# Kernel tuning notes

Measured on AMD Instinct MI355X. Metric: run time of the kernel, lower is better.

The kernel has to match this reference:

```python
import jax, jax.numpy as jnp
import numpy as np

N_NODES = 100000
N_EDGES = 1600000
NODE_NF = 11   # num_node_fs
EDGE_NF = 4    # edges_nf
H_NF = 128     # h_nf
EMB_NF = 4     # emb_nf


def _linear_params(k, fan_in, fan_out):
    # torch nn.Linear default init: U(-1/sqrt(fan_in), 1/sqrt(fan_in))
    lim = 1.0 / np.sqrt(fan_in)
    kw, kb = jax.random.split(k)
    W = jax.random.uniform(kw, (fan_in, fan_out), minval=-lim, maxval=lim, dtype=jnp.float32)
    b = jax.random.uniform(kb, (fan_out,), minval=-lim, maxval=lim, dtype=jnp.float32)
    return W, b


def setup_inputs() -> dict:
    key = jax.random.key(0)
    ks = jax.random.split(key, 8)
    node_feats = jax.random.normal(ks[0], (N_NODES, NODE_NF), dtype=jnp.float32)
    edge_index = jax.random.randint(ks[1], (2, N_EDGES), 0, N_NODES, dtype=jnp.int32)
    edge_attr = jax.random.normal(ks[2], (N_EDGES, EDGE_NF), dtype=jnp.float32)
    # NELayer edge MLP: Linear(2*in_nf+edges_nf, h_nf) -> ReLU -> Linear(h_nf, h_nf) -> ReLU
    eW1, eb1 = _linear_params(ks[3], 2 * NODE_NF + EDGE_NF, H_NF)
    eW2, eb2 = _linear_params(ks[4], H_NF, H_NF)
    # NELayer node MLP: Linear(in_nf+h_nf, h_nf) -> ReLU -> Linear(h_nf, out_nf=h_nf)
    nW1, nb1 = _linear_params(ks[5], NODE_NF + H_NF, H_NF)
    nW2, nb2 = _linear_params(ks[6], H_NF, H_NF)
    # fc_emb: Linear(h_nf, emb_nf)
    fW, fb = _linear_params(ks[7], H_NF, EMB_NF)
    return dict(node_feats=node_feats, edge_index=edge_index, edge_attr=edge_attr,
                eW1=eW1, eb1=eb1, eW2=eW2, eb2=eb2,
                nW1=nW1, nb1=nb1, nW2=nW2, nb2=nb2, fW=fW, fb=fb)


def reference(node_feats, edge_index, edge_attr,
              eW1, eb1, eW2, eb2, nW1, nb1, nW2, nb2, fW, fb):
    row, col = edge_index[0], edge_index[1]          # [E], [E]
    src = node_feats[row]                            # [E, NODE_NF] gather
    dst = node_feats[col]                            # [E, NODE_NF] gather
    # edge model
    e_in = jnp.concatenate([src, dst, edge_attr], axis=1)   # [E, 2*NODE_NF+EDGE_NF]
    e_h = jax.nn.relu(e_in @ eW1 + eb1)
    edge_feats = jax.nn.relu(e_h @ eW2 + eb2)                # [E, H_NF]
    # node model: scatter-sum edge feats to source nodes
    agg = jax.ops.segment_sum(edge_feats, row, num_segments=node_feats.shape[0])  # [N, H_NF]
    n_in = jnp.concatenate([node_feats, agg], axis=1)        # [N, NODE_NF+H_NF]
    n_h = jax.nn.relu(n_in @ nW1 + nb1)
    h = n_h @ nW2 + nb2                                      # [N, H_NF]
    # embedding head
    return h @ fW + fb                                       # [N, EMB_NF]
```

## Files before the change

kernel.cpp:

```cpp
#include <hip/hip_runtime.h>

#define N_NODES 100000
#define N_EDGES 1600000
#define NODE_NF 11
#define EDGE_NF 4
#define H_NF 128
#define SCAN_B 1024
#define NBLK ((N_NODES + SCAN_B - 1) / SCAN_B)

#define ASP 32
#define K1P 40
#define K2P 136
#define EFP 131
#define K1N 160

typedef _Float16 half8 __attribute__((ext_vector_type(8)));
typedef float floatx4 __attribute__((ext_vector_type(4)));

__device__ inline half8 load8f(const float* p) {
    float4 x0 = *(const float4*)(p);
    float4 x1 = *(const float4*)(p + 4);
    half8 r;
    r[0]=(_Float16)x0.x; r[1]=(_Float16)x0.y; r[2]=(_Float16)x0.z; r[3]=(_Float16)x0.w;
    r[4]=(_Float16)x1.x; r[5]=(_Float16)x1.y; r[6]=(_Float16)x1.z; r[7]=(_Float16)x1.w;
    return r;
}
__device__ inline half8 zero8() {
    half8 z;
    #pragma unroll
    for (int j = 0; j < 8; ++j) z[j] = (_Float16)0.f;
    return z;
}

#define SEG0 (N_NODES * 12)
#define SEG1 (SEG0 + H_NF * K1P)
#define SEG2 (SEG1 + H_NF * K2P)
#define SEG3 (SEG2 + H_NF * K1N)
#define SEG4 (SEG3 + 16 * K2P + 4)
#define SEG5 (SEG4 + N_EDGES)

__global__ __launch_bounds__(256)
void prep_hist_kernel(const float* __restrict__ nf,
                      const float* __restrict__ eW1,
                      const float* __restrict__ eW2,
                      const float* __restrict__ nW1,
                      const float* __restrict__ nW2,
                      const float* __restrict__ fW,
                      const float* __restrict__ nb2,
                      const float* __restrict__ fb,
                      const int*   __restrict__ edge_index,
                      _Float16* __restrict__ nfh,
                      _Float16* __restrict__ w1h,
                      _Float16* __restrict__ w2h,
                      _Float16* __restrict__ w1nh,
                      _Float16* __restrict__ w23h,
                      float* __restrict__ b23,
                      int* hist)
{
    int i = blockIdx.x * 256 + threadIdx.x;
    if (i < SEG0) {
        int n = i / 12, k = i - n * 12;
        nfh[i] = (k < NODE_NF) ? (_Float16)nf[(size_t)n * NODE_NF + k] : (_Float16)0.f;
    } else if (i < SEG1) {
        int j = i - SEG0;
        int n = j / K1P, k = j - n * K1P;
        float v = 0.f;
        if (k < 11)                 v = eW1[k * H_NF + n];
        else if (k >= 12 && k < 23) v = eW1[(k - 1) * H_NF + n];
        else if (k >= 24 && k < 28) v = eW1[(k - 2) * H_NF + n];
        w1h[j] = (_Float16)v;
    } else if (i < SEG2) {
        int j = i - SEG1;
        int n = j / K2P, k = j - n * K2P;
        w2h[j] = (k < H_NF) ? (_Float16)eW2[k * H_NF + n] : (_Float16)0.f;
    } else if (i < SEG3) {
        int j = i - SEG2;
        int n = j / K1N, k = j - n * K1N;
        float v = 0.f;
        if (k < 11)                  v = nW1[k * H_NF + n];
        else if (k >= 12 && k < 140) v = nW1[(k - 1) * H_NF + n];
        w1nh[j] = (_Float16)v;
    } else if (i < SEG4) {
        int j = i - SEG3;
        if (j < 16 * K2P) {
            int n = j / K2P, k = j - n * K2P;
            float v = 0.f;
            if (n < 4 && k < H_NF) {
                for (int q = 0; q < H_NF; ++q) v += nW2[k * H_NF + q] * fW[q * 4 + n];
            }
            w23h[j] = (_Float16)v;
        } else {
            int o = j - 16 * K2P;
            float v = fb[o];
            for (int q = 0; q < H_NF; ++q) v += nb2[q] * fW[q * 4 + o];
            b23[o] = v;
        }
    } else if (i < SEG5) {
        int e = i - SEG4;
        atomicAdd(&hist[edge_index[e]], 1);
    }
}

__global__ __launch_bounds__(256)
void transpose_w2(const float* __restrict__ W, float* __restrict__ WT) {
    int i = blockIdx.x * 256 + threadIdx.x;
    if (i < H_NF * H_NF) {
        int k = i >> 7, j = i & (H_NF - 1);
        WT[j * H_NF + k] = W[i];
    }
}

__global__ __launch_bounds__(SCAN_B)
void scan1_kernel(const int* __restrict__ hist, int* starts, int* bsum) {
    __shared__ int buf[SCAN_B];
    int i = blockIdx.x * SCAN_B + threadIdx.x;
    int v = (i < N_NODES) ? hist[i] : 0;
    buf[threadIdx.x] = v;
    __syncthreads();
    for (int off = 1; off < SCAN_B; off <<= 1) {
        int t = (threadIdx.x >= off) ? buf[threadIdx.x - off] : 0;
        __syncthreads();
        buf[threadIdx.x] += t;
        __syncthreads();
    }
    if (i < N_NODES) starts[i] = buf[threadIdx.x] - v;
    if (threadIdx.x == SCAN_B - 1) bsum[blockIdx.x] = buf[SCAN_B - 1];
}

__global__ void scan2_kernel(int* bsum) {
    if (threadIdx.x == 0 && blockIdx.x == 0) {
        int run = 0;
        for (int b = 0; b < NBLK; ++b) { int t = bsum[b]; bsum[b] = run; run += t; }
        bsum[NBLK] = run;
    }
}

__global__ __launch_bounds__(256)
void scan3_kernel(int* starts, int* cursor, const int* __restrict__ bsum) {
    int i = blockIdx.x * 256 + threadIdx.x;
    if (i < N_NODES) {
        int s = starts[i] + bsum[i / SCAN_B];
        starts[i] = s;
        cursor[i] = s;
    }
    if (i == 0) starts[N_NODES] = bsum[NBLK];
}

__global__ __launch_bounds__(256)
void permgather_kernel(const int* __restrict__ edge_index,
                       const _Float16* __restrict__ nfh,
                       const float* __restrict__ edge_attr,
                       int* cursor,
                       _Float16* __restrict__ Asort,
                       int* __restrict__ rows_sorted)
{
    int e = blockIdx.x * 256 + threadIdx.x;
    if (e >= N_EDGES) return;
    int row = edge_index[e];
    int col = edge_index[N_EDGES + e];
    int pos = atomicAdd(&cursor[row], 1);
    rows_sorted[pos] = row;
    const int2* ps = (const int2*)(nfh + (size_t)row * 12);
    const int2* pd = (const int2*)(nfh + (size_t)col * 12);
    int2 s0 = ps[0], s1 = ps[1], s2 = ps[2];
    int2 d0 = pd[0], d1 = pd[1], d2 = pd[2];
    float4 a4 = ((const float4*)edge_attr)[e];
    union { _Float16 h[4]; int2 v; } u;
    u.h[0] = (_Float16)a4.x; u.h[1] = (_Float16)a4.y;
    u.h[2] = (_Float16)a4.z; u.h[3] = (_Float16)a4.w;
    int2* op = (int2*)(Asort + (size_t)pos * ASP);
    op[0] = s0; op[1] = s1; op[2] = s2;
    op[3] = d0; op[4] = d1; op[5] = d2;
    op[6] = u.v; op[7] = make_int2(0, 0);
}

__global__ __launch_bounds__(256)
void permute_kernel(const int* __restrict__ edge_index, int* cursor, int* perm) {
    int e = blockIdx.x * 256 + threadIdx.x;
    if (e < N_EDGES) {
        int pos = atomicAdd(&cursor[edge_index[e]], 1);
        perm[pos] = e;
    }
}

#define E_ARENA_SZ 4480

__global__ __launch_bounds__(256, 2)
void edge_mfma_kernel(const _Float16* __restrict__ Asort,
                      const int*   __restrict__ rows_sorted,
                      const _Float16* __restrict__ w1h,
                      const float* __restrict__ eb1,
                      const _Float16* __restrict__ w2h,
                      const float* __restrict__ eb2,
                      float* agg)
{
    __shared__ __align__(16) char smem[4 * E_ARENA_SZ];
    int t = threadIdx.x;
    int wv = t >> 6, lane = t & 63;
    char* arena = smem + wv * E_ARENA_SZ;
    _Float16* Hs = (_Float16*)arena;
    int* rowsS = (int*)(arena + 4352);
    int m = lane & 15, quad = lane >> 4;

    half8 w1f[8], w2f[8][4];
    #pragma unroll
    for (int tile = 0; tile < 8; ++tile)
        w1f[tile] = *(const half8*)(w1h + (tile * 16 + m) * K1P + quad * 8);
    #pragma unroll
    for (int tile = 0; tile < 8; ++tile)
        #pragma unroll
        for (int ks = 0; ks < 4; ++ks)
            w2f[tile][ks] = *(const half8*)(w2h + (tile * 16 + m) * K2P + ks * 32 + quad * 8);
    float b1v[8], b2v[8];
    #pragma unroll
    for (int tile = 0; tile < 8; ++tile) {
        b1v[tile] = eb1[tile * 16 + m];
        b2v[tile] = eb2[tile * 16 + m];
    }

    const int nwin = N_EDGES / 16;
    const int STRIDE = gridDim.x * 4;
    int win = blockIdx.x * 4 + wv;
    if (win >= nwin) return;

    half8 a1 = *(const half8*)(Asort + (size_t)win * (16 * ASP) + m * ASP + quad * 8);
    int rs = (quad == 3) ? rows_sorted[win * 16 + m] : 0;

    while (true) {
        int next = win + STRIDE;
        bool hn = next < nwin;
        if (quad == 3) rowsS[m] = rs;
        half8 a1n = {};
        int rsn = 0;
        if (hn) {
            a1n = *(const half8*)(Asort + (size_t)next * (16 * ASP) + m * ASP + quad * 8);
            if (quad == 3) rsn = rows_sorted[next * 16 + m];
        }

        #pragma unroll
        for (int tile = 0; tile < 8; ++tile) {
            floatx4 c = {0.f, 0.f, 0.f, 0.f};
            c = __builtin_amdgcn_mfma_f32_16x16x32_f16(a1, w1f[tile], c, 0, 0, 0);
            int n = tile * 16 + m;
            #pragma unroll
            for (int r = 0; r < 4; ++r)
                Hs[(quad * 4 + r) * K2P + n] = (_Float16)fmaxf(c[r] + b1v[tile], 0.f);
        }

        half8 a2[4];
        #pragma unroll
        for (int ks = 0; ks < 4; ++ks)
            a2[ks] = *(const half8*)(Hs + m * K2P + ks * 32 + quad * 8);

        float vals[32];
        #pragma unroll
        for (int tile = 0; tile < 8; ++tile) {
            floatx4 c = {0.f, 0.f, 0.f, 0.f};
            #pragma unroll
            for (int ks = 0; ks < 4; ++ks)
                c = __builtin_amdgcn_mfma_f32_16x16x32_f16(a2[ks], w2f[tile][ks], c, 0, 0, 0);
            #pragma unroll
            for (int r = 0; r < 4; ++r)
                vals[tile * 4 + r] = fmaxf(c[r] + b2v[tile], 0.f);
        }

        int er0 = rowsS[quad * 4 + 0], er1 = rowsS[quad * 4 + 1];
        int er2 = rowsS[quad * 4 + 2], er3 = rowsS[quad * 4 + 3];
        int li = lane & 15;
        bool bi = (lane < 16) && ((li == 0) || (rowsS[li] != rowsS[li - 1]));
        unsigned long long bm = __ballot(bi);
        unsigned mk = (unsigned)(bm & 0xFFFFull);
        while (mk) {
            int start = __builtin_ctz(mk);
            mk &= mk - 1;
            int srow = rowsS[start];
            float s[8];
            #pragma unroll
            for (int tile = 0; tile < 8; ++tile) {
                float v = 0.f;
                if (er0 == srow) v += vals[tile * 4 + 0];
                if (er1 == srow) v += vals[tile * 4 + 1];
                if (er2 == srow) v += vals[tile * 4 + 2];
                if (er3 == srow) v += vals[tile * 4 + 3];
                s[tile] = v;
            }
            #pragma unroll
            for (int tile = 0; tile < 8; ++tile) {
                s[tile] += __shfl_xor(s[tile], 16);
                s[tile] += __shfl_xor(s[tile], 32);
            }
            if (quad == 0) {
                #pragma unroll
                for (int tile = 0; tile < 8; ++tile)
                    unsafeAtomicAdd(&agg[(size_t)srow * H_NF + tile * 16 + m], s[tile]);
            }
        }

        if (!hn) break;
        win = next; a1 = a1n; rs = rsn;
    }
}

#define G_W1      0
#define G_W2      10240
#define G_ARENA   45056
#define G_ARENA_SZ 8448
#define G_TOTAL   (G_ARENA + 4 * G_ARENA_SZ)

__global__ __launch_bounds__(256, 2)
void edge_mfma_gather_kernel(const _Float16* __restrict__ nfh,
                             const int*   __restrict__ edge_index,
                             const float* __restrict__ edge_attr,
                             const _Float16* __restrict__ w1h,
                             const float* __restrict__ eb1,
                             const _Float16* __restrict__ w2h,
                             const float* __restrict__ eb2,
                             const int*   __restrict__ perm,
                             float* agg)
{
    __shared__ __align__(16) char smem[G_TOTAL];
    _Float16* W1s = (_Float16*)(smem + G_W1);
    _Float16* W2s = (_Float16*)(smem + G_W2);
    int t = threadIdx.x;
    {
        const float4* g1 = (const float4*)w1h;
        float4* s1 = (float4*)W1s;
        for (int i = t; i < 640; i += 256) s1[i] = g1[i];
        const float4* g2 = (const float4*)w2h;
        float4* s2 = (float4*)W2s;
        for (int i = t; i < 2176; i += 256) s2[i] = g2[i];
    }
    __syncthreads();

    int wv = t >> 6, lane = t & 63;
    char* arena = smem + G_ARENA + wv * G_ARENA_SZ;
    _Float16* Ain  = (_Float16*)arena;
    _Float16* Hs   = (_Float16*)(arena + 1280);
    float*    efS  = (float*)arena;
    int*      rowsS = (int*)(arena + 8384);

    int m = lane & 15, quad = lane >> 4;
    int el = lane & 15, grp = lane >> 4;
    _Float16* arow = Ain + el * K1P;

    float b1v[8], b2v[8];
    #pragma unroll
    for (int tile = 0; tile < 8; ++tile) {
        b1v[tile] = eb1[tile * 16 + m];
        b2v[tile] = eb2[tile * 16 + m];
    }

    const int nwin = N_EDGES / 16;
    for (int win = blockIdx.x * 4 + wv; win < nwin; win += gridDim.x * 4) {
        int e = perm[win * 16 + el];
        if (grp < 2) {
            int node = edge_index[grp * N_EDGES + e];
            const int2* p = (const int2*)(nfh + (size_t)node * 12);
            int2 x0 = p[0], x1 = p[1], x2 = p[2];
            char* dst = (char*)(arow + grp * 12);
            *(int2*)(dst) = x0; *(int2*)(dst + 8) = x1; *(int2*)(dst + 16) = x2;
        } else if (grp == 2) {
            float4 a4 = ((const float4*)edge_attr)[e];
            arow[24] = (_Float16)a4.x; arow[25] = (_Float16)a4.y;
            arow[26] = (_Float16)a4.z; arow[27] = (_Float16)a4.w;
        } else {
            rowsS[el] = edge_index[e];
            *(int2*)((char*)arow + 56) = make_int2(0, 0);
        }

        half8 a1 = *(const half8*)(Ain + m * K1P + quad * 8);
        #pragma unroll
        for (int tile = 0; tile < 8; ++tile) {
            half8 b = *(const half8*)(W1s + (tile * 16 + m) * K1P + quad * 8);
            floatx4 c = {0.f, 0.f, 0.f, 0.f};
            c = __builtin_amdgcn_mfma_f32_16x16x32_f16(a1, b, c, 0, 0, 0);
            int n = tile * 16 + m;
            #pragma unroll
            for (int r = 0; r < 4; ++r)
                Hs[(quad * 4 + r) * K2P + n] = (_Float16)fmaxf(c[r] + b1v[tile], 0.f);
        }
        half8 a2[4];
        #pragma unroll
        for (int ks = 0; ks < 4; ++ks)
            a2[ks] = *(const half8*)(Hs + m * K2P + ks * 32 + quad * 8);
        #pragma unroll
        for (int tile = 0; tile < 8; ++tile) {
            floatx4 c = {0.f, 0.f, 0.f, 0.f};
            #pragma unroll
            for (int ks = 0; ks < 4; ++ks) {
                half8 b = *(const half8*)(W2s + (tile * 16 + m) * K2P + ks * 32 + quad * 8);
                c = __builtin_amdgcn_mfma_f32_16x16x32_f16(a2[ks], b, c, 0, 0, 0);
            }
            #pragma unroll
            for (int r = 0; r < 4; ++r)
                efS[(quad * 4 + r) * EFP + tile * 16 + m] = fmaxf(c[r] + b2v[tile], 0.f);
        }

        int f = lane;
        int cur = rowsS[0];
        float acc0 = efS[f], acc1 = efS[64 + f];
        #pragma unroll 1
        for (int i = 1; i < 16; ++i) {
            int r = rowsS[i];
            float v0 = efS[i * EFP + f];
            float v1 = efS[i * EFP + 64 + f];
            if (r != cur) {
                unsafeAtomicAdd(&agg[(size_t)cur * H_NF + f], acc0);
                unsafeAtomicAdd(&agg[(size_t)cur * H_NF + 64 + f], acc1);
                acc0 = v0; acc1 = v1; cur = r;
            } else { acc0 += v0; acc1 += v1; }
        }
        unsafeAtomicAdd(&agg[(size_t)cur * H_NF + f], acc0);
        unsafeAtomicAdd(&agg[(size_t)cur * H_NF + 64 + f], acc1);
    }
}

#define N_W1    0
#define N_W23   40960
#define N_HS    45312

__global__ __launch_bounds__(256, 2)
void node_mfma_kernel(const float* __restrict__ node_feats,
                      const float* __restrict__ agg,
                      const _Float16* __restrict__ w1nh,
                      const float* __restrict__ nb1,
                      const _Float16* __restrict__ w23h,
                      const float* __restrict__ b23,
                      float* __restrict__ out)
{
    __shared__ __align__(16) char smem[N_HS + 4 * 4352];
    _Float16* W1N  = (_Float16*)(smem + N_W1);
    _Float16* W23s = (_Float16*)(smem + N_W23);
    int t = threadIdx.x;
    {
        const float4* g1 = (const float4*)w1nh;
        float4* s1 = (float4*)W1N;
        for (int i = t; i < 2560; i += 256) s1[i] = g1[i];
        const float4* g2 = (const float4*)w23h;
        float4* s2 = (float4*)W23s;
        for (int i = t; i < 272; i += 256) s2[i] = g2[i];
    }
    __syncthreads();

    int wv = t >> 6, lane = t & 63;
    int m = lane & 15, quad = lane >> 4;
    _Float16* HsW = (_Float16*)(smem + N_HS + wv * 4352);
    const int ntile = (N_NODES + 63) / 64;

    float nb1v[8];
    #pragma unroll
    for (int tile = 0; tile < 8; ++tile) nb1v[tile] = nb1[tile * 16 + m];
    float b23v = (m < 4) ? b23[m] : 0.f;

    for (int ti = blockIdx.x; ti < ntile; ti += gridDim.x) {
        int nb = (ti * 4 + wv) * 16;
        if (nb >= N_NODES) continue;
        int nodeA = nb + m;
        if (nodeA >= N_NODES) nodeA = N_NODES - 1;
        const float* ag  = agg + (size_t)nodeA * H_NF;
        const float* nfp = node_feats + (size_t)nodeA * NODE_NF;

        half8 afr[5];
        if (quad == 0) {
            half8 r;
            #pragma unroll
            for (int j = 0; j < 8; ++j) r[j] = (_Float16)nfp[j];
            afr[0] = r;
            afr[4] = load8f(ag + 116);
        } else if (quad == 1) {
            half8 r;
            r[0] = (_Float16)nfp[8]; r[1] = (_Float16)nfp[9];
            r[2] = (_Float16)nfp[10]; r[3] = (_Float16)0.f;
            float4 x = *(const float4*)(ag);
            r[4] = (_Float16)x.x; r[5] = (_Float16)x.y;
            r[6] = (_Float16)x.z; r[7] = (_Float16)x.w;
            afr[0] = r;
            float4 y = *(const float4*)(ag + 124);
            half8 s = zero8();
            s[0] = (_Float16)y.x; s[1] = (_Float16)y.y;
            s[2] = (_Float16)y.z; s[3] = (_Float16)y.w;
            afr[4] = s;
        } else if (quad == 2) {
            afr[0] = load8f(ag + 4);
            afr[4] = zero8();
        } else {
            afr[0] = load8f(ag + 12);
            afr[4] = zero8();
        }
        afr[1] = load8f(ag + 20 + 8 * quad);
        afr[2] = load8f(ag + 52 + 8 * quad);
        afr[3] = load8f(ag + 84 + 8 * quad);

        #pragma unroll
        for (int tile = 0; tile < 8; ++tile) {
            floatx4 c = {0.f, 0.f, 0.f, 0.f};
            #pragma unroll
            for (int ks = 0; ks < 5; ++ks) {
                half8 b = *(const half8*)(W1N + (tile * 16 + m) * K1N + ks * 32 + quad * 8);
                c = __builtin_amdgcn_mfma_f32_16x16x32_f16(afr[ks], b, c, 0, 0, 0);
            }
            #pragma unroll
            for (int r = 0; r < 4; ++r)
                HsW[(quad * 4 + r) * K2P + tile * 16 + m] = (_Float16)fmaxf(c[r] + nb1v[tile], 0.f);
        }

        half8 a2[4];
        #pragma unroll
        for (int ks = 0; ks < 4; ++ks)
            a2[ks] = *(const half8*)(HsW + m * K2P + ks * 32 + quad * 8);
        floatx4 c23 = {0.f, 0.f, 0.f, 0.f};
        #pragma unroll
        for (int ks = 0; ks < 4; ++ks) {
            half8 b = *(const half8*)(W23s + m * K2P + ks * 32 + quad * 8);
            c23 = __builtin_amdgcn_mfma_f32_16x16x32_f16(a2[ks], b, c23, 0, 0, 0);
        }
        if (m < 4) {
            #pragma unroll
            for (int r = 0; r < 4; ++r) {
                int node = nb + quad * 4 + r;
                if (node < N_NODES) out[node * 4 + m] = c23[r] + b23v;
            }
        }
    }
}

__global__ __launch_bounds__(256)
void edge_kernel_atomic(const float* __restrict__ node_feats,
                        const int*   __restrict__ edge_index,
                        const float* __restrict__ edge_attr,
                        const float* __restrict__ eW1,
                        const float* __restrict__ eb1,
                        const float* __restrict__ W2T,
                        const float* __restrict__ eb2,
                        float* agg)
{
    int e = blockIdx.x * 256 + threadIdx.x;
    if (e >= N_EDGES) return;
    int row = edge_index[e];
    int col = edge_index[N_EDGES + e];
    float h[H_NF];
    #pragma unroll
    for (int j = 0; j < H_NF; ++j) h[j] = eb1[j];
    const float* srcp = node_feats + (size_t)row * NODE_NF;
    #pragma unroll 1
    for (int k = 0; k < NODE_NF; ++k) {
        float x = srcp[k];
        const float* w = eW1 + k * H_NF;
        #pragma unroll
        for (int j = 0; j < H_NF; ++j) h[j] = fmaf(x, w[j], h[j]);
    }
    const float* dstp = node_feats + (size_t)col * NODE_NF;
    #pragma unroll 1
    for (int k = 0; k < NODE_NF; ++k) {
        float x = dstp[k];
        const float* w = eW1 + (NODE_NF + k) * H_NF;
        #pragma unroll
        for (int j = 0; j < H_NF; ++j) h[j] = fmaf(x, w[j], h[j]);
    }
    float4 at = ((const float4*)edge_attr)[e];
    float av[EDGE_NF] = {at.x, at.y, at.z, at.w};
    #pragma unroll
    for (int k = 0; k < EDGE_NF; ++k) {
        float x = av[k];
        const float* w = eW1 + (2 * NODE_NF + k) * H_NF;
        #pragma unroll
        for (int j = 0; j < H_NF; ++j) h[j] = fmaf(x, w[j], h[j]);
    }
    #pragma unroll
    for (int j = 0; j < H_NF; ++j) h[j] = fmaxf(h[j], 0.f);
    #pragma unroll 1
    for (int j0 = 0; j0 < H_NF; j0 += 8) {
        float acc[8];
        #pragma unroll
        for (int jj = 0; jj < 8; ++jj) acc[jj] = eb2[j0 + jj];
        #pragma unroll
        for (int k = 0; k < H_NF; ++k) {
            float x = h[k];
            #pragma unroll
            for (int jj = 0; jj < 8; ++jj)
                acc[jj] = fmaf(x, W2T[(j0 + jj) * H_NF + k], acc[jj]);
        }
        #pragma unroll
        for (int jj = 0; jj < 8; ++jj)
            unsafeAtomicAdd(&agg[(size_t)row * H_NF + j0 + jj], fmaxf(acc[jj], 0.f));
    }
}

__global__ __launch_bounds__(256)
void node_kernel1(const float* __restrict__ node_feats, float* agg_nh,
                  const float* __restrict__ nW1, const float* __restrict__ nb1)
{
    int n = blockIdx.x * 256 + threadIdx.x;
    if (n >= N_NODES) return;
    float acc[H_NF];
    #pragma unroll
    for (int j = 0; j < H_NF; ++j) acc[j] = nb1[j];
    const float* nfp = node_feats + (size_t)n * NODE_NF;
    #pragma unroll 1
    for (int k = 0; k < NODE_NF; ++k) {
        float x = nfp[k];
        const float* w = nW1 + k * H_NF;
        #pragma unroll
        for (int j = 0; j < H_NF; ++j) acc[j] = fmaf(x, w[j], acc[j]);
    }
    const float4* ap = (const float4*)(agg_nh + (size_t)n * H_NF);
    #pragma unroll 1
    for (int k4 = 0; k4 < H_NF / 4; ++k4) {
        float4 x = ap[k4];
        const float* w0 = nW1 + (NODE_NF + k4 * 4 + 0) * H_NF;
        const float* w1 = nW1 + (NODE_NF + k4 * 4 + 1) * H_NF;
        const float* w2 = nW1 + (NODE_NF + k4 * 4 + 2) * H_NF;
        const float* w3 = nW1 + (NODE_NF + k4 * 4 + 3) * H_NF;
        #pragma unroll
        for (int j = 0; j < H_NF; ++j) {
            acc[j] = fmaf(x.x, w0[j], acc[j]);
            acc[j] = fmaf(x.y, w1[j], acc[j]);
            acc[j] = fmaf(x.z, w2[j], acc[j]);
            acc[j] = fmaf(x.w, w3[j], acc[j]);
        }
    }
    float* op = agg_nh + (size_t)n * H_NF;
    #pragma unroll
    for (int j4 = 0; j4 < H_NF / 4; ++j4) {
        float4 o = make_float4(fmaxf(acc[j4*4+0], 0.f), fmaxf(acc[j4*4+1], 0.f),
                               fmaxf(acc[j4*4+2], 0.f), fmaxf(acc[j4*4+3], 0.f));
        ((float4*)op)[j4] = o;
    }
}

__global__ __launch_bounds__(256)
void node_kernel2(const float* __restrict__ nh, const float* __restrict__ nW2,
                  const float* __restrict__ nb2, const float* __restrict__ fW,
                  const float* __restrict__ fb, float* __restrict__ out)
{
    int n = blockIdx.x * 256 + threadIdx.x;
    if (n >= N_NODES) return;
    float acc[H_NF];
    #pragma unroll
    for (int j = 0; j < H_NF; ++j) acc[j] = nb2[j];
    const float4* hp = (const float4*)(nh + (size_t)n * H_NF);
    #pragma unroll 1
    for (int k4 = 0; k4 < H_NF / 4; ++k4) {
        float4 x = hp[k4];
        const float* w0 = nW2 + (k4 * 4 + 0) * H_NF;
        const float* w1 = nW2 + (k4 * 4 + 1) * H_NF;
        const float* w2 = nW2 + (k4 * 4 + 2) * H_NF;
        const float* w3 = nW2 + (k4 * 4 + 3) * H_NF;
        #pragma unroll
        for (int j = 0; j < H_NF; ++j) {
            acc[j] = fmaf(x.x, w0[j], acc[j]);
            acc[j] = fmaf(x.y, w1[j], acc[j]);
            acc[j] = fmaf(x.z, w2[j], acc[j]);
            acc[j] = fmaf(x.w, w3[j], acc[j]);
        }
    }
    float o0 = fb[0], o1 = fb[1], o2 = fb[2], o3 = fb[3];
    #pragma unroll
    for (int j = 0; j < H_NF; ++j) {
        o0 = fmaf(acc[j], fW[j * 4 + 0], o0);
        o1 = fmaf(acc[j], fW[j * 4 + 1], o1);
        o2 = fmaf(acc[j], fW[j * 4 + 2], o2);
        o3 = fmaf(acc[j], fW[j * 4 + 3], o3);
    }
    ((float4*)out)[n] = make_float4(o0, o1, o2, o3);
}

extern "C" void kernel_launch(void* const* d_in, const int* in_sizes, int n_in,
                              void* d_out, int out_size, void* d_ws, size_t ws_size,
                              hipStream_t stream)
{
    const float* node_feats = (const float*)d_in[0];
    const int*   edge_index = (const int*)d_in[1];
    const float* edge_attr  = (const float*)d_in[2];
    const float* eW1 = (const float*)d_in[3];
    const float* eb1 = (const float*)d_in[4];
    const float* eW2 = (const float*)d_in[5];
    const float* eb2 = (const float*)d_in[6];
    const float* nW1 = (const float*)d_in[7];
    const float* nb1 = (const float*)d_in[8];
    const float* nW2 = (const float*)d_in[9];
    const float* nb2 = (const float*)d_in[10];
    const float* fW  = (const float*)d_in[11];
    const float* fb  = (const float*)d_in[12];
    float* out = (float*)d_out;

    size_t off = 0;
    auto carve = [&](size_t bytes) {
        void* p = (char*)d_ws + off;
        off = (off + bytes + 255) & ~(size_t)255;
        return p;
    };
    float*     agg    = (float*)carve((size_t)N_NODES * H_NF * sizeof(float));
    int*       hist   = (int*)  carve((size_t)N_NODES * sizeof(int));
    size_t zero_bytes = off;
    int*       starts = (int*)  carve((size_t)(N_NODES + 1) * sizeof(int));
    int*       cursor = (int*)  carve((size_t)N_NODES * sizeof(int));
    int*       bsum   = (int*)  carve((size_t)(NBLK + 1) * sizeof(int));
    _Float16*  nfh    = (_Float16*)carve((size_t)N_NODES * 12 * sizeof(_Float16));
    _Float16*  w1h    = (_Float16*)carve((size_t)H_NF * K1P * sizeof(_Float16));
    _Float16*  w2h    = (_Float16*)carve((size_t)H_NF * K2P * sizeof(_Float16));
    _Float16*  w1nh   = (_Float16*)carve((size_t)H_NF * K1N * sizeof(_Float16));
    _Float16*  w23h   = (_Float16*)carve((size_t)16 * K2P * sizeof(_Float16));
    float*     b23    = (float*)carve(4 * sizeof(float));
    int*       perm   = (int*)  carve((size_t)N_EDGES * sizeof(int));
    size_t required_t2 = off;
    _Float16*  Asort  = (_Float16*)carve((size_t)N_EDGES * ASP * sizeof(_Float16));
    int*       rowsS  = (int*)carve((size_t)N_EDGES * sizeof(int));
    size_t required_t1 = off;

    if (ws_size >= required_t2) {
        hipMemsetAsync(d_ws, 0, zero_bytes, stream);
        prep_hist_kernel<<<(SEG5 + 255) / 256, 256, 0, stream>>>(
            node_feats, eW1, eW2, nW1, nW2, fW, nb2, fb, edge_index,
            nfh, w1h, w2h, w1nh, w23h, b23, hist);
        scan1_kernel<<<NBLK, SCAN_B, 0, stream>>>(hist, starts, bsum);
        scan2_kernel<<<1, 64, 0, stream>>>(bsum);
        scan3_kernel<<<(N_NODES + 255) / 256, 256, 0, stream>>>(starts, cursor, bsum);

        if (ws_size >= required_t1) {
            permgather_kernel<<<(N_EDGES + 255) / 256, 256, 0, stream>>>(
                edge_index, nfh, edge_attr, cursor, Asort, rowsS);
            edge_mfma_kernel<<<512, 256, 0, stream>>>(
                Asort, rowsS, w1h, eb1, w2h, eb2, agg);
        } else {
            permute_kernel<<<(N_EDGES + 255) / 256, 256, 0, stream>>>(edge_index, cursor, perm);
            edge_mfma_gather_kernel<<<512, 256, 0, stream>>>(
                nfh, edge_index, edge_attr, w1h, eb1, w2h, eb2, perm, agg);
        }
        node_mfma_kernel<<<512, 256, 0, stream>>>(
            node_feats, agg, w1nh, nb1, w23h, b23, out);
    } else {
        float* agg_fb = (float*)d_ws;
        float* W2T_fb = (float*)((char*)d_ws + (size_t)N_NODES * H_NF * sizeof(float));
        transpose_w2<<<(H_NF * H_NF + 255) / 256, 256, 0, stream>>>(eW2, W2T_fb);
        hipMemsetAsync(agg_fb, 0, (size_t)N_NODES * H_NF * sizeof(float), stream);
        edge_kernel_atomic<<<(N_EDGES + 255) / 256, 256, 0, stream>>>(
            node_feats, edge_index, edge_attr, eW1, eb1, W2T_fb, eb2, agg_fb);
        node_kernel1<<<(N_NODES + 255) / 256, 256, 0, stream>>>(node_feats, agg_fb, nW1, nb1);
        node_kernel2<<<(N_NODES + 255) / 256, 256, 0, stream>>>(agg_fb, nW2, nb2, fW, fb, out);
    }
}
```

Baseline: 474.3 us.

## Sort compact edge records and gather node features inside edge MFMA kernel

The permutation kernel now writes a 16-byte record (row, col, fp16 edge attrs) per sorted edge instead of a 64-byte pre-gathered fp16 input row plus a separate sorted-row array. The edge MFMA kernel gathers source and destination node features from the small fp16 node table itself, software-prefetching the next window's records and features, and assembles the A tile in LDS. Row ids for segment detection are taken from registers with shuffles instead of LDS. This cuts intermediate write and read traffic but moves random gathers into the compute kernel, where their latency may be exposed, and adds an LDS round-trip per window.

```diff
diff --git a/kernel.cpp b/kernel.cpp
--- a/kernel.cpp
+++ b/kernel.cpp
@@ -8,7 +8,6 @@
 #define SCAN_B 1024
 #define NBLK ((N_NODES + SCAN_B - 1) / SCAN_B)
 
-#define ASP 32
 #define K1P 40
 #define K2P 136
 #define EFP 131
@@ -147,31 +146,21 @@
 }
 
 __global__ __launch_bounds__(256)
-void permgather_kernel(const int* __restrict__ edge_index,
-                       const _Float16* __restrict__ nfh,
-                       const float* __restrict__ edge_attr,
-                       int* cursor,
-                       _Float16* __restrict__ Asort,
-                       int* __restrict__ rows_sorted)
+void permrec_kernel(const int* __restrict__ edge_index,
+                    const float* __restrict__ edge_attr,
+                    int* cursor,
+                    int4* __restrict__ rec)
 {
     int e = blockIdx.x * 256 + threadIdx.x;
     if (e >= N_EDGES) return;
     int row = edge_index[e];
     int col = edge_index[N_EDGES + e];
-    int pos = atomicAdd(&cursor[row], 1);
-    rows_sorted[pos] = row;
-    const int2* ps = (const int2*)(nfh + (size_t)row * 12);
-    const int2* pd = (const int2*)(nfh + (size_t)col * 12);
-    int2 s0 = ps[0], s1 = ps[1], s2 = ps[2];
-    int2 d0 = pd[0], d1 = pd[1], d2 = pd[2];
     float4 a4 = ((const float4*)edge_attr)[e];
     union { _Float16 h[4]; int2 v; } u;
     u.h[0] = (_Float16)a4.x; u.h[1] = (_Float16)a4.y;
     u.h[2] = (_Float16)a4.z; u.h[3] = (_Float16)a4.w;
-    int2* op = (int2*)(Asort + (size_t)pos * ASP);
-    op[0] = s0; op[1] = s1; op[2] = s2;
-    op[3] = d0; op[4] = d1; op[5] = d2;
-    op[6] = u.v; op[7] = make_int2(0, 0);
+    int pos = atomicAdd(&cursor[row], 1);
+    rec[pos] = make_int4(row, col, u.v.x, u.v.y);
 }
 
 __global__ __launch_bounds__(256)
@@ -183,11 +172,11 @@
     }
 }
 
-#define E_ARENA_SZ 4480
+#define E_ARENA_SZ 5504
 
 __global__ __launch_bounds__(256, 2)
-void edge_mfma_kernel(const _Float16* __restrict__ Asort,
-                      const int*   __restrict__ rows_sorted,
+void edge_mfma_kernel(const int4* __restrict__ recs,
+                      const _Float16* __restrict__ nfh,
                       const _Float16* __restrict__ w1h,
                       const float* __restrict__ eb1,
                       const _Float16* __restrict__ w2h,
@@ -198,8 +187,8 @@
     int t = threadIdx.x;
     int wv = t >> 6, lane = t & 63;
     char* arena = smem + wv * E_ARENA_SZ;
-    _Float16* Hs = (_Float16*)arena;
-    int* rowsS = (int*)(arena + 4352);
+    _Float16* Ain = (_Float16*)arena;
+    _Float16* Hs  = (_Float16*)(arena + 1024);
     int m = lane & 15, quad = lane >> 4;
 
     half8 w1f[8], w2f[8][4];
@@ -223,19 +212,33 @@
     int win = blockIdx.x * 4 + wv;
     if (win >= nwin) return;
 
-    half8 a1 = *(const half8*)(Asort + (size_t)win * (16 * ASP) + m * ASP + quad * 8);
-    int rs = (quad == 3) ? rows_sorted[win * 16 + m] : 0;
+    int4 rc = recs[win * 16 + m];
+    int2 g0 = make_int2(0, 0), g1 = g0, g2 = g0;
+    if (quad < 2) {
+        int node = (quad == 0) ? rc.x : rc.y;
+        const int2* p = (const int2*)(nfh + (size_t)node * 12);
+        g0 = p[0]; g1 = p[1]; g2 = p[2];
+    }
 
     while (true) {
         int next = win + STRIDE;
         bool hn = next < nwin;
-        if (quad == 3) rowsS[m] = rs;
-        half8 a1n = {};
-        int rsn = 0;
-        if (hn) {
-            a1n = *(const half8*)(Asort + (size_t)next * (16 * ASP) + m * ASP + quad * 8);
-            if (quad == 3) rsn = rows_sorted[next * 16 + m];
-        }
+        int4 rcn = make_int4(0, 0, 0, 0);
+        if (hn) rcn = recs[next * 16 + m];
+
+        _Float16* arow = Ain + m * 32;
+        if (quad == 0) {
+            ((int2*)arow)[0] = g0; ((int2*)arow)[1] = g1; ((int2*)arow)[2] = g2;
+        } else if (quad == 1) {
+            int2* d = (int2*)(arow + 12);
+            d[0] = g0; d[1] = g1; d[2] = g2;
+        } else if (quad == 2) {
+            int2* d = (int2*)(arow + 24);
+            d[0] = make_int2(rc.z, rc.w);
+            d[1] = make_int2(0, 0);
+        }
+
+        half8 a1 = *(const half8*)(Ain + m * 32 + quad * 8);
 
         #pragma unroll
         for (int tile = 0; tile < 8; ++tile) {
@@ -264,16 +267,26 @@
                 vals[tile * 4 + r] = fmaxf(c[r] + b2v[tile], 0.f);
         }
 
-        int er0 = rowsS[quad * 4 + 0], er1 = rowsS[quad * 4 + 1];
-        int er2 = rowsS[quad * 4 + 2], er3 = rowsS[quad * 4 + 3];
-        int li = lane & 15;
-        bool bi = (lane < 16) && ((li == 0) || (rowsS[li] != rowsS[li - 1]));
+        int2 n0 = make_int2(0, 0), n1 = n0, n2 = n0;
+        if (hn && quad < 2) {
+            int node = (quad == 0) ? rcn.x : rcn.y;
+            const int2* p = (const int2*)(nfh + (size_t)node * 12);
+            n0 = p[0]; n1 = p[1]; n2 = p[2];
+        }
+
+        int row = rc.x;
+        int rprev = __shfl(row, lane - 1);
+        bool bi = (lane < 16) && (m == 0 || rprev != row);
         unsigned long long bm = __ballot(bi);
         unsigned mk = (unsigned)(bm & 0xFFFFull);
+        int er0 = __shfl(row, quad * 4 + 0);
+        int er1 = __shfl(row, quad * 4 + 1);
+        int er2 = __shfl(row, quad * 4 + 2);
+        int er3 = __shfl(row, quad * 4 + 3);
         while (mk) {
             int start = __builtin_ctz(mk);
             mk &= mk - 1;
-            int srow = rowsS[start];
+            int srow = __shfl(row, start);
             float s[8];
             #pragma unroll
             for (int tile = 0; tile < 8; ++tile) {
@@ -297,7 +310,7 @@
         }
 
         if (!hn) break;
-        win = next; a1 = a1n; rs = rsn;
+        win = next; rc = rcn; g0 = n0; g1 = n1; g2 = n2;
     }
 }
 
@@ -704,8 +717,7 @@
     float*     b23    = (float*)carve(4 * sizeof(float));
     int*       perm   = (int*)  carve((size_t)N_EDGES * sizeof(int));
     size_t required_t2 = off;
-    _Float16*  Asort  = (_Float16*)carve((size_t)N_EDGES * ASP * sizeof(_Float16));
-    int*       rowsS  = (int*)carve((size_t)N_EDGES * sizeof(int));
+    int4*      rec    = (int4*) carve((size_t)N_EDGES * sizeof(int4));
     size_t required_t1 = off;
 
     if (ws_size >= required_t2) {
@@ -718,10 +730,10 @@
         scan3_kernel<<<(N_NODES + 255) / 256, 256, 0, stream>>>(starts, cursor, bsum);
 
         if (ws_size >= required_t1) {
-            permgather_kernel<<<(N_EDGES + 255) / 256, 256, 0, stream>>>(
-                edge_index, nfh, edge_attr, cursor, Asort, rowsS);
+            permrec_kernel<<<(N_EDGES + 255) / 256, 256, 0, stream>>>(
+                edge_index, edge_attr, cursor, rec);
             edge_mfma_kernel<<<512, 256, 0, stream>>>(
-                Asort, rowsS, w1h, eb1, w2h, eb2, agg);
+                rec, nfh, w1h, eb1, w2h, eb2, agg);
         } else {
             permute_kernel<<<(N_EDGES + 255) / 256, 256, 0, stream>>>(edge_index, cursor, perm);
             edge_mfma_gather_kernel<<<512, 256, 0, stream>>>(
```

After: 424.2 us. 10.6% less time.
